# Kernel optimization log

Measured on AMD Instinct MI355X. Metric: run time of the kernel, lower is better.

The kernel has to match this reference:

```python
import jax, jax.numpy as jnp
import numpy as np

N_NODES = 100000
N_EDGES = 1600000
IN_FEATS = 128
H_FEATS = 64
PROP_STEP = 2


def _gcn_propagate(x, src, dst, num_nodes, add_self_loops):
    """PyG gcn_norm + scatter-add propagation. edge_weight=None -> all ones.
    GCNConv uses add_self_loops=True; LGConv uses add_self_loops=False."""
    if add_self_loops:
        loop = jnp.arange(num_nodes, dtype=src.dtype)
        src = jnp.concatenate([src, loop])
        dst = jnp.concatenate([dst, loop])
    # degree over destination nodes (flow source_to_target)
    deg = jax.ops.segment_sum(jnp.ones(src.shape, dtype=x.dtype), dst,
                              num_segments=num_nodes)
    dinv = jnp.where(deg > 0, jax.lax.rsqrt(deg), jnp.zeros_like(deg))
    norm = dinv[src] * dinv[dst]                      # [E]
    msg = x[src] * norm[:, None]                      # [E, F] gather + scale
    return jax.ops.segment_sum(msg, dst, num_segments=num_nodes)  # [N, F]


def setup_inputs() -> dict:
    key = jax.random.key(0)
    k1, k2, k3 = jax.random.split(key, 3)
    edge_index = jax.random.randint(k1, (2, N_EDGES), 0, N_NODES, dtype=jnp.int32)
    in_feat = jax.random.normal(k2, (N_NODES, IN_FEATS), dtype=jnp.float32)
    # GCNConv linear weight (bias=False), stored as [in, out]
    W1 = jax.random.normal(k3, (IN_FEATS, H_FEATS), dtype=jnp.float32) * (1.0 / np.sqrt(IN_FEATS))
    alphas = jnp.ones((PROP_STEP,), dtype=jnp.float32)  # nn.Parameter(ones(prop_step))
    return {"edge_index": edge_index, "in_feat": in_feat, "W1": W1, "alphas": alphas}


def reference(edge_index, in_feat, W1, alphas):
    src, dst = edge_index[0], edge_index[1]
    num_nodes = in_feat.shape[0]
    alpha = jax.nn.softmax(alphas)
    # conv1 = GCNConv(bias=False): linear transform then normalized propagation with self loops
    h = _gcn_propagate(in_feat @ W1, src, dst, num_nodes, add_self_loops=True)
    res = h * alpha[0]
    # remaining steps: LGConv (no self loops), norm/relu disabled by default
    for i in range(1, PROP_STEP):
        h = _gcn_propagate(h, src, dst, num_nodes, add_self_loops=False)
        res = res + h * alpha[i]
    return res
```

## Files before the change

### kernel.cpp

```cpp
#include <hip/hip_runtime.h>

#define N_NODES 100000
#define N_EDGES 1600000
#define IN_F 128
#define H_F 64
#define ZROW N_NODES

#define BSH 10
#define BNODES 1024
#define NBKT 98
#define EPB 4096
#define BCAP 20000

typedef short short8 __attribute__((ext_vector_type(8)));
typedef float floatx4 __attribute__((ext_vector_type(4)));

union U16x8 { short8 v; unsigned short us[8]; unsigned int u[4]; };

static __device__ __forceinline__ unsigned short f2bf(float f) {
    unsigned int u = __float_as_uint(f);
    unsigned int r = (u + 0x7FFFu + ((u >> 16) & 1u)) >> 16;
    return (unsigned short)r;
}
static __device__ __forceinline__ float bf2f(unsigned short v) {
    return __uint_as_float(((unsigned int)v) << 16);
}
static __device__ __forceinline__ float bflo(unsigned int u) {
    return __uint_as_float(u << 16);
}
static __device__ __forceinline__ float bfhi(unsigned int u) {
    return __uint_as_float(u & 0xFFFF0000u);
}
static __device__ __forceinline__ unsigned int pk2(float a, float b) {
    return (unsigned int)f2bf(a) | ((unsigned int)f2bf(b) << 16);
}

__global__ __launch_bounds__(256) void initwpack_kernel(const float* __restrict__ W,
                                                        unsigned int* __restrict__ wfrag,
                                                        int* __restrict__ ccur,
                                                        int* __restrict__ offsets,
                                                        unsigned int* __restrict__ XsZ,
                                                        unsigned int* __restrict__ h1sZ) {
    int i = blockIdx.x * 256 + threadIdx.x;
    int reg = i & 3, lane = (i >> 2) & 63, fkc = i >> 8;
    int ct = fkc >> 2, kc = fkc & 3;
    int fcol = ct * 16 + (lane & 15);
    int k = kc * 32 + (lane >> 4) * 8 + reg * 2;
    wfrag[i] = pk2(W[k * 64 + fcol], W[(k + 1) * 64 + fcol]);

    if (blockIdx.x == 0) {
        int t = threadIdx.x;
        if (t < NBKT) ccur[t] = t * BCAP;
        if (t == 0) offsets[N_NODES] = N_EDGES;
        if (t < 32) XsZ[t] = 0;
        else if (t < 64) h1sZ[t - 32] = 0;
    }
}

__global__ __launch_bounds__(256) void coarse_scatter_kernel(const int* __restrict__ src,
                                                             const int* __restrict__ dst,
                                                             int* __restrict__ ccur,
                                                             unsigned int* __restrict__ tmp, int E) {
    __shared__ unsigned int buf[EPB];
    __shared__ unsigned char bktA[EPB];
    __shared__ int cnt[NBKT], lofs[NBKT], gofs[NBKT];
    int base = blockIdx.x * EPB;
    int n = E - base; if (n > EPB) n = EPB;

    for (int i = threadIdx.x; i < NBKT; i += 256) cnt[i] = 0;
    __syncthreads();

    unsigned int v[16]; int bk[16], loc[16];
    #pragma unroll
    for (int j = 0; j < 16; ++j) {
        int o = threadIdx.x + j * 256;
        bk[j] = -1;
        if (o < n) {
            int s = src[base + o];
            int d = dst[base + o];
            bk[j]  = d >> BSH;
            v[j]   = ((unsigned int)(d & (BNODES - 1)) << 17) | (unsigned int)s;
            loc[j] = atomicAdd(&cnt[bk[j]], 1);
        }
    }
    __syncthreads();
    if (threadIdx.x == 0) {
        int run = 0;
        for (int b = 0; b < NBKT; ++b) { lofs[b] = run; run += cnt[b]; }
    }
    __syncthreads();
    if (threadIdx.x < NBKT && cnt[threadIdx.x] > 0)
        gofs[threadIdx.x] = atomicAdd(&ccur[threadIdx.x], cnt[threadIdx.x]);
    __syncthreads();
    #pragma unroll
    for (int j = 0; j < 16; ++j)
        if (bk[j] >= 0) {
            int p = lofs[bk[j]] + loc[j];
            buf[p]  = v[j];
            bktA[p] = (unsigned char)bk[j];
        }
    __syncthreads();
    for (int i = threadIdx.x; i < n; i += 256) {
        int b = bktA[i];
        tmp[gofs[b] + (i - lofs[b])] = buf[i];
    }
}

__global__ __launch_bounds__(512) void bucket_kernel(const unsigned int* __restrict__ tmp,
                                                     const int* __restrict__ ccur,
                                                     int* __restrict__ offsets,
                                                     int* __restrict__ sorted_src,
                                                     float* __restrict__ dinv1,
                                                     float* __restrict__ dinv2, int N) {
    __shared__ int cnt[BNODES];
    __shared__ int sd[512];
    __shared__ int obase_s;
    int b   = blockIdx.x;
    int tid = threadIdx.x;
    int tbeg = b * BCAP, tend = ccur[b];

    if (tid == 0) {
        int run = 0;
        for (int q = 0; q < b; ++q) run += ccur[q] - q * BCAP;
        obase_s = run;
    }
    for (int i = tid; i < BNODES; i += 512) cnt[i] = 0;
    __syncthreads();
    for (int i = tbeg + tid; i < tend; i += 512)
        atomicAdd(&cnt[tmp[i] >> 17], 1);
    __syncthreads();

    int c0 = cnt[2 * tid], c1 = cnt[2 * tid + 1];
    int s  = c0 + c1;
    sd[tid] = s;
    __syncthreads();
    for (int off = 1; off < 512; off <<= 1) {
        int t = (tid >= off) ? sd[tid - off] : 0;
        __syncthreads();
        sd[tid] += t;
        __syncthreads();
    }
    int obase = obase_s;
    int ex = sd[tid] - s;
    int g0 = obase + ex, g1 = obase + ex + c0;

    int node0 = b * BNODES + 2 * tid;
    if (node0 < N) {
        offsets[node0] = g0;
        dinv1[node0] = rsqrtf((float)(c0 + 1));
        dinv2[node0] = c0 ? rsqrtf((float)c0) : 0.0f;
    }
    if (node0 + 1 < N) {
        offsets[node0 + 1] = g1;
        dinv1[node0 + 1] = rsqrtf((float)(c1 + 1));
        dinv2[node0 + 1] = c1 ? rsqrtf((float)c1) : 0.0f;
    }
    __syncthreads();
    cnt[2 * tid] = g0;
    cnt[2 * tid + 1] = g1;
    __syncthreads();

    for (int i = tbeg + tid; i < tend; i += 512) {
        unsigned int v = tmp[i];
        int p = atomicAdd(&cnt[v >> 17], 1);
        sorted_src[p] = (int)(v & 0x1FFFFu);
    }
}

__global__ __launch_bounds__(256) void gemm_kernel(const float* __restrict__ A,
                                                   const uint4* __restrict__ wfrag,
                                                   const float* __restrict__ dinv1,
                                                   unsigned short* __restrict__ Xs, int nTiles) {
    int wid = blockIdx.x * 4 + (threadIdx.x >> 6);
    int lane = threadIdx.x & 63;
    int lrow = lane & 15, lk = lane >> 4;

    short8 wf[16];
    #pragma unroll
    for (int i = 0; i < 16; ++i)
        wf[i] = *reinterpret_cast<const short8*>(&wfrag[i * 64 + lane]);

    #pragma unroll
    for (int tt = 0; tt < 4; ++tt) {
        int t = wid * 4 + tt;
        if (t >= nTiles) break;
        int node = t * 16 + lrow;
        const float4* ap = reinterpret_cast<const float4*>(A + (size_t)node * IN_F);

        short8 af[4];
        #pragma unroll
        for (int kc = 0; kc < 4; ++kc) {
            float4 x = ap[kc * 8 + lk * 2];
            float4 y = ap[kc * 8 + lk * 2 + 1];
            U16x8 u;
            u.us[0] = f2bf(x.x); u.us[1] = f2bf(x.y); u.us[2] = f2bf(x.z); u.us[3] = f2bf(x.w);
            u.us[4] = f2bf(y.x); u.us[5] = f2bf(y.y); u.us[6] = f2bf(y.z); u.us[7] = f2bf(y.w);
            af[kc] = u.v;
        }

        float dv = dinv1[node];
        #pragma unroll
        for (int ct = 0; ct < 4; ++ct) {
            floatx4 acc = {0.f, 0.f, 0.f, 0.f};
            acc = __builtin_amdgcn_mfma_f32_16x16x32_bf16(wf[ct * 4 + 0], af[0], acc, 0, 0, 0);
            acc = __builtin_amdgcn_mfma_f32_16x16x32_bf16(wf[ct * 4 + 1], af[1], acc, 0, 0, 0);
            acc = __builtin_amdgcn_mfma_f32_16x16x32_bf16(wf[ct * 4 + 2], af[2], acc, 0, 0, 0);
            acc = __builtin_amdgcn_mfma_f32_16x16x32_bf16(wf[ct * 4 + 3], af[3], acc, 0, 0, 0);
            uint2 o;
            o.x = pk2(acc[0] * dv, acc[1] * dv);
            o.y = pk2(acc[2] * dv, acc[3] * dv);
            *reinterpret_cast<uint2*>(Xs + (size_t)node * H_F + ct * 16 + lk * 4) = o;
        }
    }
}

__global__ __launch_bounds__(256) void prop1_kernel(const int* __restrict__ offsets,
                                                    const int* __restrict__ sorted_src,
                                                    const unsigned short* __restrict__ Xs,
                                                    const float* __restrict__ dinv1,
                                                    const float* __restrict__ dinv2,
                                                    unsigned short* __restrict__ h1,
                                                    unsigned short* __restrict__ h1s, int N) {
    int wid  = (blockIdx.x * blockDim.x + threadIdx.x) >> 6;
    int lane = threadIdx.x & 63;
    int g = lane >> 4, fl = lane & 15;
    int d = wid * 4 + g;
    bool active = d < N;
    int dd = active ? d : N - 1;

    int beg = offsets[dd], end = offsets[dd + 1];
    int gb = g << 4;
    float c0 = 0.f, c1 = 0.f, c2 = 0.f, c3 = 0.f;

    for (int i0 = beg; i0 < end; i0 += 16) {
        int lim = end - i0;
        int s_l = (fl < lim) ? sorted_src[i0 + fl] : ZROW;
        uint2 v[16];
        #pragma unroll
        for (int j = 0; j < 16; ++j) {
            int s = __shfl(s_l, gb + j);
            v[j] = *reinterpret_cast<const uint2*>(Xs + ((size_t)s << 6) + (fl << 2));
        }
        #pragma unroll
        for (int j = 0; j < 16; ++j) {
            c0 += bflo(v[j].x); c1 += bfhi(v[j].x); c2 += bflo(v[j].y); c3 += bfhi(v[j].y);
        }
    }

    float dv  = dinv1[dd];
    float dv2 = dinv2[dd];
    uint2 sv = *reinterpret_cast<const uint2*>(Xs + ((size_t)dd << 6) + (fl << 2));
    float h0  = dv * (c0 + bflo(sv.x));
    float h1v = dv * (c1 + bfhi(sv.x));
    float h2  = dv * (c2 + bflo(sv.y));
    float h3  = dv * (c3 + bfhi(sv.y));
    if (active) {
        uint2 o1; o1.x = pk2(h0, h1v); o1.y = pk2(h2, h3);
        *reinterpret_cast<uint2*>(h1 + ((size_t)d << 6) + (fl << 2)) = o1;
        uint2 o2; o2.x = pk2(h0 * dv2, h1v * dv2); o2.y = pk2(h2 * dv2, h3 * dv2);
        *reinterpret_cast<uint2*>(h1s + ((size_t)d << 6) + (fl << 2)) = o2;
    }
}

__global__ __launch_bounds__(256) void prop2_kernel(const int* __restrict__ offsets,
                                                    const int* __restrict__ sorted_src,
                                                    const unsigned short* __restrict__ h1,
                                                    const unsigned short* __restrict__ h1s,
                                                    const float* __restrict__ dinv2,
                                                    const float* __restrict__ alphas,
                                                    float* __restrict__ out, int N) {
    int wid  = (blockIdx.x * blockDim.x + threadIdx.x) >> 6;
    int lane = threadIdx.x & 63;
    int g = lane >> 4, fl = lane & 15;
    int d = wid * 4 + g;
    bool active = d < N;
    int dd = active ? d : N - 1;

    float e0 = expf(alphas[0]), e1 = expf(alphas[1]);
    float aw0 = e0 / (e0 + e1), aw1 = e1 / (e0 + e1);

    int beg = offsets[dd], end = offsets[dd + 1];
    int gb = g << 4;
    float c0 = 0.f, c1 = 0.f, c2 = 0.f, c3 = 0.f;

    for (int i0 = beg; i0 < end; i0 += 16) {
        int lim = end - i0;
        int s_l = (fl < lim) ? sorted_src[i0 + fl] : ZROW;
        uint2 v[16];
        #pragma unroll
        for (int j = 0; j < 16; ++j) {
            int s = __shfl(s_l, gb + j);
            v[j] = *reinterpret_cast<const uint2*>(h1s + ((size_t)s << 6) + (fl << 2));
        }
        #pragma unroll
        for (int j = 0; j < 16; ++j) {
            c0 += bflo(v[j].x); c1 += bfhi(v[j].x); c2 += bflo(v[j].y); c3 += bfhi(v[j].y);
        }
    }

    if (active) {
        float sa1 = aw1 * dinv2[dd];
        uint2 sv = *reinterpret_cast<const uint2*>(h1 + ((size_t)d << 6) + (fl << 2));
        float4 o;
        o.x = aw0 * bflo(sv.x) + sa1 * c0;
        o.y = aw0 * bfhi(sv.x) + sa1 * c1;
        o.z = aw0 * bflo(sv.y) + sa1 * c2;
        o.w = aw0 * bfhi(sv.y) + sa1 * c3;
        *reinterpret_cast<float4*>(out + ((size_t)d << 6) + (fl << 2)) = o;
    }
}

extern "C" void kernel_launch(void* const* d_in, const int* in_sizes, int n_in,
                              void* d_out, int out_size, void* d_ws, size_t ws_size,
                              hipStream_t stream) {
    const int*   edge_index = (const int*)d_in[0];
    const float* in_feat    = (const float*)d_in[1];
    const float* W1         = (const float*)d_in[2];
    const float* alphas     = (const float*)d_in[3];
    float*       out        = (float*)d_out;

    const int* src = edge_index;
    const int* dst = edge_index + N_EDGES;

    char* ws = (char*)d_ws;
    size_t tabBytes = (size_t)(N_NODES + 16) * H_F * 2;
    unsigned short* Xs  = (unsigned short*)(ws);
    unsigned int*   tmp = (unsigned int*)(ws);
    unsigned short* h1  = (unsigned short*)(ws + tabBytes);
    unsigned short* h1s = (unsigned short*)(ws + 2 * tabBytes);
    char* p = ws + 3 * tabBytes;
    int*   sorted = (int*)p;   p += (size_t)N_EDGES * 4;
    int*   offs   = (int*)p;   p += (size_t)(N_NODES + 4) * 4;
    float* dinv1  = (float*)p; p += (size_t)N_NODES * 4;
    float* dinv2  = (float*)p; p += (size_t)N_NODES * 4;
    int*   ccur   = (int*)p;   p += (size_t)NBKT * 4;
    unsigned int* wfrag = (unsigned int*)p; p += 8192 * 4;

    initwpack_kernel<<<32, 256, 0, stream>>>(W1, wfrag, ccur, offs,
                                             (unsigned int*)(Xs + (size_t)N_NODES * H_F),
                                             (unsigned int*)(h1s + (size_t)N_NODES * H_F));
    coarse_scatter_kernel<<<(N_EDGES + EPB - 1) / EPB, 256, 0, stream>>>(src, dst, ccur, tmp, N_EDGES);
    bucket_kernel<<<NBKT, 512, 0, stream>>>(tmp, ccur, offs, sorted, dinv1, dinv2, N_NODES);

    int nTiles = N_NODES / 16;
    int gemm_waves = (nTiles + 3) / 4;
    gemm_kernel<<<(gemm_waves + 3) / 4, 256, 0, stream>>>(in_feat, (const uint4*)wfrag, dinv1, Xs, nTiles);

    int pwaves  = (N_NODES + 3) / 4;
    int pblocks = (pwaves + 3) / 4;
    prop1_kernel<<<pblocks, 256, 0, stream>>>(offs, sorted, Xs, dinv1, dinv2, h1, h1s, N_NODES);
    prop2_kernel<<<pblocks, 256, 0, stream>>>(offs, sorted, h1, h1s, dinv2, alphas, out, N_NODES);
}
```

Measured before the change: 131.4 us.

## Pad per-node CSR neighbor lists to multiples of eight with zero-row sentinels

The bucket kernel now places each bucket at a fixed slot region and pads every node's neighbor list to a multiple of 8 with indices to a zero row, storing the padded chunk count per node. This drops the serial prefix over earlier buckets. The propagation kernels become simpler: each lane loads 8 indices directly and gathers 8 rows per iteration, with no shuffle broadcast and no bounds check, which cuts per-edge overhead and shortens the tail of each loop. The cost is extra padded gathers of the zero row, a larger sorted array, and redundant per-lane index loads.

New measurement: 129.4 us (median of 2 runs). No clear change (-1.5%).

```diff
diff --git a/kernel.cpp b/kernel.cpp
--- a/kernel.cpp
+++ b/kernel.cpp
@@ -11,6 +11,7 @@
 #define NBKT 98
 #define EPB 4096
 #define BCAP 20000
+#define SCAP 28192
 
 typedef short short8 __attribute__((ext_vector_type(8)));
 typedef float floatx4 __attribute__((ext_vector_type(4)));
@@ -22,9 +23,6 @@
     unsigned int r = (u + 0x7FFFu + ((u >> 16) & 1u)) >> 16;
     return (unsigned short)r;
 }
-static __device__ __forceinline__ float bf2f(unsigned short v) {
-    return __uint_as_float(((unsigned int)v) << 16);
-}
 static __device__ __forceinline__ float bflo(unsigned int u) {
     return __uint_as_float(u << 16);
 }
@@ -38,7 +36,6 @@
 __global__ __launch_bounds__(256) void initwpack_kernel(const float* __restrict__ W,
                                                         unsigned int* __restrict__ wfrag,
                                                         int* __restrict__ ccur,
-                                                        int* __restrict__ offsets,
                                                         unsigned int* __restrict__ XsZ,
                                                         unsigned int* __restrict__ h1sZ) {
     int i = blockIdx.x * 256 + threadIdx.x;
@@ -51,7 +48,6 @@
     if (blockIdx.x == 0) {
         int t = threadIdx.x;
         if (t < NBKT) ccur[t] = t * BCAP;
-        if (t == 0) offsets[N_NODES] = N_EDGES;
         if (t < 32) XsZ[t] = 0;
         else if (t < 64) h1sZ[t - 32] = 0;
     }
@@ -109,21 +105,17 @@
 __global__ __launch_bounds__(512) void bucket_kernel(const unsigned int* __restrict__ tmp,
                                                      const int* __restrict__ ccur,
                                                      int* __restrict__ offsets,
+                                                     unsigned char* __restrict__ npad8,
                                                      int* __restrict__ sorted_src,
                                                      float* __restrict__ dinv1,
                                                      float* __restrict__ dinv2, int N) {
     __shared__ int cnt[BNODES];
     __shared__ int sd[512];
-    __shared__ int obase_s;
     int b   = blockIdx.x;
     int tid = threadIdx.x;
     int tbeg = b * BCAP, tend = ccur[b];
-
-    if (tid == 0) {
-        int run = 0;
-        for (int q = 0; q < b; ++q) run += ccur[q] - q * BCAP;
-        obase_s = run;
-    }
+    int sbase = b * SCAP;
+
     for (int i = tid; i < BNODES; i += 512) cnt[i] = 0;
     __syncthreads();
     for (int i = tbeg + tid; i < tend; i += 512)
@@ -131,7 +123,8 @@
     __syncthreads();
 
     int c0 = cnt[2 * tid], c1 = cnt[2 * tid + 1];
-    int s  = c0 + c1;
+    int p0 = (c0 + 7) & ~7, p1 = (c1 + 7) & ~7;
+    int s  = p0 + p1;
     sd[tid] = s;
     __syncthreads();
     for (int off = 1; off < 512; off <<= 1) {
@@ -140,20 +133,23 @@
         sd[tid] += t;
         __syncthreads();
     }
-    int obase = obase_s;
     int ex = sd[tid] - s;
-    int g0 = obase + ex, g1 = obase + ex + c0;
+    int g0 = sbase + ex, g1 = sbase + ex + p0;
 
     int node0 = b * BNODES + 2 * tid;
     if (node0 < N) {
         offsets[node0] = g0;
+        npad8[node0] = (unsigned char)(p0 >> 3);
         dinv1[node0] = rsqrtf((float)(c0 + 1));
         dinv2[node0] = c0 ? rsqrtf((float)c0) : 0.0f;
+        for (int k = c0; k < p0; ++k) sorted_src[g0 + k] = ZROW;
     }
     if (node0 + 1 < N) {
         offsets[node0 + 1] = g1;
+        npad8[node0 + 1] = (unsigned char)(p1 >> 3);
         dinv1[node0 + 1] = rsqrtf((float)(c1 + 1));
         dinv2[node0 + 1] = c1 ? rsqrtf((float)c1) : 0.0f;
+        for (int k = c1; k < p1; ++k) sorted_src[g1 + k] = ZROW;
     }
     __syncthreads();
     cnt[2 * tid] = g0;
@@ -215,6 +211,7 @@
 }
 
 __global__ __launch_bounds__(256) void prop1_kernel(const int* __restrict__ offsets,
+                                                    const unsigned char* __restrict__ npad8,
                                                     const int* __restrict__ sorted_src,
                                                     const unsigned short* __restrict__ Xs,
                                                     const float* __restrict__ dinv1,
@@ -228,28 +225,29 @@
     bool active = d < N;
     int dd = active ? d : N - 1;
 
-    int beg = offsets[dd], end = offsets[dd + 1];
-    int gb = g << 4;
+    int beg = offsets[dd];
+    int nit = npad8[dd];
+    const int* idp = sorted_src + beg;
+    const char* XsB = (const char*)Xs;
+    unsigned bo = (unsigned)(fl << 3);
     float c0 = 0.f, c1 = 0.f, c2 = 0.f, c3 = 0.f;
 
-    for (int i0 = beg; i0 < end; i0 += 16) {
-        int lim = end - i0;
-        int s_l = (fl < lim) ? sorted_src[i0 + fl] : ZROW;
-        uint2 v[16];
-        #pragma unroll
-        for (int j = 0; j < 16; ++j) {
-            int s = __shfl(s_l, gb + j);
-            v[j] = *reinterpret_cast<const uint2*>(Xs + ((size_t)s << 6) + (fl << 2));
-        }
-        #pragma unroll
-        for (int j = 0; j < 16; ++j) {
+    for (int it = 0; it < nit; ++it, idp += 8) {
+        int s[8]; uint2 v[8];
+        #pragma unroll
+        for (int j = 0; j < 8; ++j) s[j] = idp[j];
+        #pragma unroll
+        for (int j = 0; j < 8; ++j)
+            v[j] = *reinterpret_cast<const uint2*>(XsB + (((unsigned)s[j] << 7) + bo));
+        #pragma unroll
+        for (int j = 0; j < 8; ++j) {
             c0 += bflo(v[j].x); c1 += bfhi(v[j].x); c2 += bflo(v[j].y); c3 += bfhi(v[j].y);
         }
     }
 
     float dv  = dinv1[dd];
     float dv2 = dinv2[dd];
-    uint2 sv = *reinterpret_cast<const uint2*>(Xs + ((size_t)dd << 6) + (fl << 2));
+    uint2 sv = *reinterpret_cast<const uint2*>(XsB + (((unsigned)dd << 7) + bo));
     float h0  = dv * (c0 + bflo(sv.x));
     float h1v = dv * (c1 + bfhi(sv.x));
     float h2  = dv * (c2 + bflo(sv.y));
@@ -263,6 +261,7 @@
 }
 
 __global__ __launch_bounds__(256) void prop2_kernel(const int* __restrict__ offsets,
+                                                    const unsigned char* __restrict__ npad8,
                                                     const int* __restrict__ sorted_src,
                                                     const unsigned short* __restrict__ h1,
                                                     const unsigned short* __restrict__ h1s,
@@ -279,28 +278,29 @@
     float e0 = expf(alphas[0]), e1 = expf(alphas[1]);
     float aw0 = e0 / (e0 + e1), aw1 = e1 / (e0 + e1);
 
-    int beg = offsets[dd], end = offsets[dd + 1];
-    int gb = g << 4;
+    int beg = offsets[dd];
+    int nit = npad8[dd];
+    const int* idp = sorted_src + beg;
+    const char* HB = (const char*)h1s;
+    unsigned bo = (unsigned)(fl << 3);
     float c0 = 0.f, c1 = 0.f, c2 = 0.f, c3 = 0.f;
 
-    for (int i0 = beg; i0 < end; i0 += 16) {
-        int lim = end - i0;
-        int s_l = (fl < lim) ? sorted_src[i0 + fl] : ZROW;
-        uint2 v[16];
-        #pragma unroll
-        for (int j = 0; j < 16; ++j) {
-            int s = __shfl(s_l, gb + j);
-            v[j] = *reinterpret_cast<const uint2*>(h1s + ((size_t)s << 6) + (fl << 2));
-        }
-        #pragma unroll
-        for (int j = 0; j < 16; ++j) {
+    for (int it = 0; it < nit; ++it, idp += 8) {
+        int s[8]; uint2 v[8];
+        #pragma unroll
+        for (int j = 0; j < 8; ++j) s[j] = idp[j];
+        #pragma unroll
+        for (int j = 0; j < 8; ++j)
+            v[j] = *reinterpret_cast<const uint2*>(HB + (((unsigned)s[j] << 7) + bo));
+        #pragma unroll
+        for (int j = 0; j < 8; ++j) {
             c0 += bflo(v[j].x); c1 += bfhi(v[j].x); c2 += bflo(v[j].y); c3 += bfhi(v[j].y);
         }
     }
 
     if (active) {
         float sa1 = aw1 * dinv2[dd];
-        uint2 sv = *reinterpret_cast<const uint2*>(h1 + ((size_t)d << 6) + (fl << 2));
+        uint2 sv = *reinterpret_cast<const uint2*>((const char*)h1 + (((unsigned)d << 7) + bo));
         float4 o;
         o.x = aw0 * bflo(sv.x) + sa1 * c0;
         o.y = aw0 * bfhi(sv.x) + sa1 * c1;
@@ -329,18 +329,20 @@
     unsigned short* h1  = (unsigned short*)(ws + tabBytes);
     unsigned short* h1s = (unsigned short*)(ws + 2 * tabBytes);
     char* p = ws + 3 * tabBytes;
-    int*   sorted = (int*)p;   p += (size_t)N_EDGES * 4;
+    int*   sorted = (int*)p;   p += (size_t)NBKT * SCAP * 4;
     int*   offs   = (int*)p;   p += (size_t)(N_NODES + 4) * 4;
     float* dinv1  = (float*)p; p += (size_t)N_NODES * 4;
     float* dinv2  = (float*)p; p += (size_t)N_NODES * 4;
+    unsigned char* npad8 = (unsigned char*)p; p += (size_t)(N_NODES + 64);
+    p = (char*)(((size_t)p + 63) & ~(size_t)63);
     int*   ccur   = (int*)p;   p += (size_t)NBKT * 4;
     unsigned int* wfrag = (unsigned int*)p; p += 8192 * 4;
 
-    initwpack_kernel<<<32, 256, 0, stream>>>(W1, wfrag, ccur, offs,
+    initwpack_kernel<<<32, 256, 0, stream>>>(W1, wfrag, ccur,
                                              (unsigned int*)(Xs + (size_t)N_NODES * H_F),
                                              (unsigned int*)(h1s + (size_t)N_NODES * H_F));
     coarse_scatter_kernel<<<(N_EDGES + EPB - 1) / EPB, 256, 0, stream>>>(src, dst, ccur, tmp, N_EDGES);
-    bucket_kernel<<<NBKT, 512, 0, stream>>>(tmp, ccur, offs, sorted, dinv1, dinv2, N_NODES);
+    bucket_kernel<<<NBKT, 512, 0, stream>>>(tmp, ccur, offs, npad8, sorted, dinv1, dinv2, N_NODES);
 
     int nTiles = N_NODES / 16;
     int gemm_waves = (nTiles + 3) / 4;
@@ -348,6 +350,6 @@
 
     int pwaves  = (N_NODES + 3) / 4;
     int pblocks = (pwaves + 3) / 4;
-    prop1_kernel<<<pblocks, 256, 0, stream>>>(offs, sorted, Xs, dinv1, dinv2, h1, h1s, N_NODES);
-    prop2_kernel<<<pblocks, 256, 0, stream>>>(offs, sorted, h1, h1s, dinv2, alphas, out, N_NODES);
-}
+    prop1_kernel<<<pblocks, 256, 0, stream>>>(offs, npad8, sorted, Xs, dinv1, dinv2, h1, h1s, N_NODES);
+    prop2_kernel<<<pblocks, 256, 0, stream>>>(offs, npad8, sorted, h1, h1s, dinv2, alphas, out, N_NODES);
+}
```
